# Kernel tuning notes

Measured on AMD Instinct MI355X. Metric: run time of the kernel, lower is better.

The kernel has to match this reference:

```python
import jax, jax.numpy as jnp
import numpy as np

N = 100000
E = 1600000
D = 64


def setup_inputs() -> dict:
    key = jax.random.key(0)
    ks = jax.random.split(key, 10)
    x = jax.random.normal(ks[0], (N, D), dtype=jnp.float32)
    edge_index = jax.random.randint(ks[1], (2, E), 0, N, dtype=jnp.int64)
    edge_weight = jax.random.uniform(ks[2], (E,), dtype=jnp.float32)
    s = 1.0 / np.sqrt(D)
    # GraphConv params: lin_rel (with bias) applied to aggregated messages,
    # lin_root (no bias) applied to the node's own features.
    W_rel1 = jax.random.uniform(ks[3], (D, D), jnp.float32, -s, s)
    b_rel1 = jax.random.uniform(ks[4], (D,), jnp.float32, -s, s)
    W_root1 = jax.random.uniform(ks[5], (D, D), jnp.float32, -s, s)
    W_rel2 = jax.random.uniform(ks[6], (D, D), jnp.float32, -s, s)
    b_rel2 = jax.random.uniform(ks[7], (D,), jnp.float32, -s, s)
    W_root2 = jax.random.uniform(ks[8], (D, D), jnp.float32, -s, s)
    return {"x": x, "edge_index": edge_index, "edge_weight": edge_weight,
            "W_rel1": W_rel1, "b_rel1": b_rel1, "W_root1": W_root1,
            "W_rel2": W_rel2, "b_rel2": b_rel2, "W_root2": W_root2}


def _graph_conv(x, src, dst, ew, W_rel, b_rel, W_root):
    # message: x_j * e_ji, scatter-add at target node i (edge_index[1])
    msg = x[src] * ew[:, None]                                   # [E, D]
    agg = jax.ops.segment_sum(msg, dst, num_segments=x.shape[0])  # [N, D]
    return agg @ W_rel.T + b_rel + x @ W_root.T


def reference(x, edge_index, edge_weight, W_rel1, b_rel1, W_root1, W_rel2, b_rel2, W_root2):
    src, dst = edge_index[0], edge_index[1]
    h = _graph_conv(x, src, dst, edge_weight, W_rel1, b_rel1, W_root1)
    h = jax.nn.relu(h)
    h = _graph_conv(h, src, dst, edge_weight, W_rel2, b_rel2, W_root2)
    return h  # final ReLU dropped (layers[:-1])
```

## Files before the change

kernel.cpp:

```cpp
#include <hip/hip_runtime.h>
#include <hip/hip_bf16.h>
#include <stdint.h>


#define D 64
#define EPB   2048
#define EPT   4
#define NBMAX 256
#define CAPB  10240
#define GW 8
#define GR 4
#define AW 8

typedef unsigned int   u32;
typedef unsigned short u16;

__device__ __forceinline__ float bf2f(u16 v) {
    return __uint_as_float(((u32)v) << 16);
}
__device__ __forceinline__ u16 f2bf(float f) {
    u32 u = __float_as_uint(f);
    u32 r = (u + 0x7fffu + ((u >> 16) & 1u)) >> 16;
    return (u16)r;
}

__global__ __launch_bounds__(512) void binA_kernel(
    const int* __restrict__ ei, const float* __restrict__ ew,
    int* __restrict__ bucketCnt, uint64_t* __restrict__ bucketBuf, int E_, int nb)
{
    __shared__ uint64_t lds_e[EPB];
    __shared__ int lcnt[NBMAX];
    __shared__ int loff[NBMAX];
    __shared__ int gbase[NBMAX];

    int tid  = threadIdx.x;
    int tile = blockIdx.x * EPB;
    int cnt  = min(EPB, E_ - tile);
    if (cnt <= 0) return;

    for (int k = tid; k < nb; k += 512) lcnt[k] = 0;
    __syncthreads();

    bool     val[EPT];
    int      lp[EPT], bk[EPT];
    uint64_t ent[EPT];
#pragma unroll
    for (int j = 0; j < EPT; ++j) {
        int l = j * 512 + tid;
        val[j] = (l < cnt);
        if (val[j]) {
            int e   = tile + l;
            int src = ei[e];
            int dst = ei[E_ + e];
            u32 wb  = (u32)f2bf(ew[e]) & 0x7FFFu;
            u32 p32 = ((u32)src << 15) | wb;
            int b   = dst >> 9;
            ent[j] = ((uint64_t)(u32)dst << 32) | p32;
            bk[j]  = b;
            lp[j]  = atomicAdd(&lcnt[b], 1);
        }
    }
    __syncthreads();

    if (tid == 0) {
        int run = 0;
        for (int b = 0; b < nb; ++b) { int c = lcnt[b]; loff[b] = run; run += c; }
    }
    __syncthreads();
    if (tid < nb) gbase[tid] = atomicAdd(&bucketCnt[tid], lcnt[tid]);
    __syncthreads();

#pragma unroll
    for (int j = 0; j < EPT; ++j)
        if (val[j]) lds_e[loff[bk[j]] + lp[j]] = ent[j];
    __syncthreads();

    for (int k = tid; k < cnt; k += 512) {
        uint64_t en = lds_e[k];
        int b   = (int)(en >> 41);
        int gp  = gbase[b] + (k - loff[b]);
        if (gp < CAPB)
            bucketBuf[(size_t)b * CAPB + gp] = en;
    }
}

__global__ __launch_bounds__(256) void degscan_kernel(
    const uint64_t* __restrict__ bucketBuf, const int* __restrict__ bucketCnt,
    int* __restrict__ loc, int* __restrict__ bucketTot, int nb, int Nn)
{
    __shared__ int ldeg[512];
    __shared__ int wsum[4];
    int b = blockIdx.x;
    if (b >= nb) return;
    int node0 = b << 9;
    int tid = threadIdx.x;
    for (int k = tid; k < 512; k += 256) ldeg[k] = 0;
    __syncthreads();

    int cnt = min(bucketCnt[b], CAPB);
    for (int k = tid; k < cnt; k += 256)
        atomicAdd(&ldeg[((int)(bucketBuf[(size_t)b * CAPB + k] >> 32)) - node0], 1);
    __syncthreads();

    int v0 = ldeg[2 * tid], v1 = ldeg[2 * tid + 1];
    int s = v0 + v1;
    int lane = tid & 63, wave = tid >> 6;
    int inc = s;
    for (int off = 1; off < 64; off <<= 1) {
        int u = __shfl_up(inc, off);
        if (lane >= off) inc += u;
    }
    if (lane == 63) wsum[wave] = inc;
    __syncthreads();
    int woff = 0;
    for (int w2 = 0; w2 < wave; ++w2) woff += wsum[w2];
    int ex = woff + inc - s;
    int n0 = node0 + 2 * tid;
    if (n0 < Nn)     loc[n0]     = ex;
    if (n0 + 1 < Nn) loc[n0 + 1] = ex + v0;
    if (tid == 255) bucketTot[b] = woff + inc;
}

__global__ __launch_bounds__(1024) void scan2_kernel(int* __restrict__ partial, int nchunk)
{
    __shared__ int sd[1024];
    int t = threadIdx.x;
    if (t < nchunk) sd[t] = partial[t];
    __syncthreads();
    if (t == 0) {
        int run = 0;
        for (int i = 0; i < nchunk; ++i) { int v = sd[i]; sd[i] = run; run += v; }
    }
    __syncthreads();
    if (t < nchunk) partial[t] = sd[t];
}

__global__ __launch_bounds__(256) void binB2_kernel(
    const uint64_t* __restrict__ bucketBuf, const int* __restrict__ bucketCnt,
    const int* __restrict__ loc, const int* __restrict__ partial,
    int* __restrict__ rowptr, u32* __restrict__ pairs, int nb, int Nn, int E_)
{
    __shared__ int lcur[512];
    int b = blockIdx.x;
    if (b >= nb) return;
    int node0 = b << 9;
    int tid = threadIdx.x;
    int base = partial[b];
    for (int k = tid; k < 512; k += 256) {
        int node = node0 + k;
        if (node < Nn) {
            int v = loc[node] + base;
            lcur[k] = v;
            rowptr[node] = v;
        }
    }
    if (b == nb - 1 && tid == 0) rowptr[Nn] = E_;
    __syncthreads();

    int cnt = min(bucketCnt[b], CAPB);
    for (int k = tid; k < cnt; k += 256) {
        uint64_t en = bucketBuf[(size_t)b * CAPB + k];
        int dst = (int)(en >> 32);
        int p = atomicAdd(&lcur[dst - node0], 1);
        pairs[p] = (u32)en;
    }
}

__global__ __launch_bounds__(512) void gemm_kernel(
    const float* xin,
    const float* __restrict__ Wrel, const float* __restrict__ brel,
    const float* __restrict__ Wroot,
    u16* __restrict__ xr, float* io, int Nn)
{
    __shared__ float WrelT[D][D + 1];
    __shared__ float WrootT[D][D + 1];
    __shared__ float bias[D];
    __shared__ float rowX[GW][GR][D];

    int tid = threadIdx.x;
    for (int i = tid; i < D * D; i += 512) {
        int d = i >> 6, k = i & 63;
        WrelT [k][d] = Wrel [i];
        WrootT[k][d] = Wroot[i];
    }
    if (tid < D) bias[tid] = brel[tid];
    __syncthreads();

    int wave = tid >> 6, lane = tid & 63;

    int base = (blockIdx.x * GW + wave) * GR;
    if (base >= Nn) return;
    int nr = min(GR, Nn - base);

    for (int r = 0; r < nr; ++r)
        rowX[wave][r][lane] = xin[(size_t)(base + r) * D + lane];

    float aR[GR] = {0.f, 0.f, 0.f, 0.f};
    float aC[GR] = {0.f, 0.f, 0.f, 0.f};
#pragma unroll
    for (int k4 = 0; k4 < 16; ++k4) {
        float4 xv[GR];
#pragma unroll
        for (int r = 0; r < GR; ++r)
            xv[r] = *reinterpret_cast<const float4*>(&rowX[wave][r][k4 * 4]);
#pragma unroll
        for (int kk = 0; kk < 4; ++kk) {
            float wr = WrelT [k4 * 4 + kk][lane];
            float wc = WrootT[k4 * 4 + kk][lane];
#pragma unroll
            for (int r = 0; r < GR; ++r) {
                float xk = (kk == 0) ? xv[r].x : (kk == 1) ? xv[r].y
                         : (kk == 2) ? xv[r].z : xv[r].w;
                aR[r] = fmaf(xk, wr, aR[r]);
                aC[r] = fmaf(xk, wc, aC[r]);
            }
        }
    }
    for (int r = 0; r < nr; ++r) {
        size_t o = (size_t)(base + r) * D + lane;
        xr[o] = f2bf(aR[r]);
        io[o] = aC[r] + bias[lane];
    }
}

__global__ __launch_bounds__(512) void gather1_fused(
    const u16* __restrict__ xr1, const u32* __restrict__ pairs,
    const int* __restrict__ rowptr,
    const float* __restrict__ Wrel, const float* __restrict__ brel,
    const float* __restrict__ Wroot,
    u16* __restrict__ xr2, float* __restrict__ io, int Nn)
{
    __shared__ float WrelT[D][D + 1];
    __shared__ float WrootT[D][D + 1];
    __shared__ float bias[D];
    __shared__ float rowH[GW][2][D];

    int tid = threadIdx.x;
    for (int i2 = tid; i2 < D * D; i2 += 512) {
        int d = i2 >> 6, k = i2 & 63;
        WrelT [k][d] = Wrel [i2];
        WrootT[k][d] = Wroot[i2];
    }
    if (tid < D) bias[tid] = brel[tid];
    __syncthreads();

    int wave = tid >> 6, lane = tid & 63;
    int i0 = ((int)blockIdx.x * GW + wave) * 2;
    if (i0 >= Nn) return;
    int i1 = i0 + 1;
    bool row1v = (i1 < Nn);
    int i1c = row1v ? i1 : i0;

    int beg0 = __builtin_amdgcn_readfirstlane(rowptr[i0]);
    int end0 = __builtin_amdgcn_readfirstlane(rowptr[i0 + 1]);
    int beg1 = __builtin_amdgcn_readfirstlane(rowptr[i1c]);
    int end1 = __builtin_amdgcn_readfirstlane(rowptr[i1c + 1]);
    int deg0 = end0 - beg0;
    int deg1 = row1v ? (end1 - beg1) : 0;
    int dmax = max(deg0, deg1);

    int half = lane >> 5;
    int c    = lane & 31;

    float a00 = 0.f, a01 = 0.f, a10 = 0.f, a11 = 0.f;
    for (int b = 0; b < dmax; b += 16) {
#pragma unroll
        for (int jj = 0; jj < 8; ++jj) {
            int j0 = b + 2 * jj;
            u32 q0 = pairs[beg0 + j0];
            u32 q1 = pairs[beg0 + j0 + 1];
            int   s00 = (j0     < deg0) ? (int)(q0 >> 15) : 0;
            float w00 = (j0     < deg0) ? __uint_as_float((q0 & 0x7FFFu) << 16) : 0.f;
            int   s01 = (j0 + 1 < deg0) ? (int)(q1 >> 15) : 0;
            float w01 = (j0 + 1 < deg0) ? __uint_as_float((q1 & 0x7FFFu) << 16) : 0.f;
            int   sa  = half ? s01 : s00;
            float wa  = half ? w01 : w00;
            u32 va = *reinterpret_cast<const u32*>(xr1 + (size_t)sa * D + c * 2);
            u32 r0 = pairs[beg1 + j0];
            u32 r1 = pairs[beg1 + j0 + 1];
            int   s10 = (j0     < deg1) ? (int)(r0 >> 15) : 0;
            float w10 = (j0     < deg1) ? __uint_as_float((r0 & 0x7FFFu) << 16) : 0.f;
            int   s11 = (j0 + 1 < deg1) ? (int)(r1 >> 15) : 0;
            float w11 = (j0 + 1 < deg1) ? __uint_as_float((r1 & 0x7FFFu) << 16) : 0.f;
            int   sb  = half ? s11 : s10;
            float wb  = half ? w11 : w10;
            u32 vb = *reinterpret_cast<const u32*>(xr1 + (size_t)sb * D + c * 2);

            a00 = fmaf(__uint_as_float(va << 16),          wa, a00);
            a01 = fmaf(__uint_as_float(va & 0xFFFF0000u),  wa, a01);
            a10 = fmaf(__uint_as_float(vb << 16),          wb, a10);
            a11 = fmaf(__uint_as_float(vb & 0xFFFF0000u),  wb, a11);
        }
    }
    a00 += __shfl_xor(a00, 32);
    a01 += __shfl_xor(a01, 32);
    a10 += __shfl_xor(a10, 32);
    a11 += __shfl_xor(a11, 32);

    if (half == 0)
        *reinterpret_cast<float2*>(&rowH[wave][0][c * 2]) = make_float2(a00, a01);
    else
        *reinterpret_cast<float2*>(&rowH[wave][1][c * 2]) = make_float2(a10, a11);

    size_t o0 = (size_t)i0 * D + lane;
    float h0 = fmaxf(rowH[wave][0][lane] + io[o0], 0.f);
    rowH[wave][0][lane] = h0;
    size_t o1 = (size_t)i1c * D + lane;
    float h1 = fmaxf(rowH[wave][1][lane] + io[o1], 0.f);
    rowH[wave][1][lane] = h1;

#pragma unroll
    for (int r = 0; r < 2; ++r) {
        if (r == 1 && !row1v) break;
        const float4* rH4 = reinterpret_cast<const float4*>(rowH[wave][r]);
        float aR = 0.f;
        float aC = bias[lane];
#pragma unroll
        for (int k4 = 0; k4 < 16; ++k4) {
            float4 hv = rH4[k4];
            int k = k4 * 4;
            aR = fmaf(hv.x, WrelT [k + 0][lane], aR);
            aR = fmaf(hv.y, WrelT [k + 1][lane], aR);
            aR = fmaf(hv.z, WrelT [k + 2][lane], aR);
            aR = fmaf(hv.w, WrelT [k + 3][lane], aR);
            aC = fmaf(hv.x, WrootT[k + 0][lane], aC);
            aC = fmaf(hv.y, WrootT[k + 1][lane], aC);
            aC = fmaf(hv.z, WrootT[k + 2][lane], aC);
            aC = fmaf(hv.w, WrootT[k + 3][lane], aC);
        }
        size_t o = (size_t)(i0 + r) * D + lane;
        xr2[o] = f2bf(aR);
        io[o]  = aC;
    }
}

__global__ __launch_bounds__(512) void gather2_kernel(
    const u16* __restrict__ xr, const u32* __restrict__ pairs,
    const int* __restrict__ rowptr, float* __restrict__ io, int Nn)
{
    int tid  = threadIdx.x;
    int wave = tid >> 6, lane = tid & 63;
    int i0 = ((int)blockIdx.x * AW + wave) * 2;
    if (i0 >= Nn) return;
    int i1 = i0 + 1;
    bool row1v = (i1 < Nn);
    int i1c = row1v ? i1 : i0;

    int beg0 = __builtin_amdgcn_readfirstlane(rowptr[i0]);
    int end0 = __builtin_amdgcn_readfirstlane(rowptr[i0 + 1]);
    int beg1 = __builtin_amdgcn_readfirstlane(rowptr[i1c]);
    int end1 = __builtin_amdgcn_readfirstlane(rowptr[i1c + 1]);
    int deg0 = end0 - beg0;
    int deg1 = row1v ? (end1 - beg1) : 0;
    int dmax = max(deg0, deg1);

    int half = lane >> 5;
    int c    = lane & 31;

    float a00 = 0.f, a01 = 0.f, a10 = 0.f, a11 = 0.f;
    for (int b = 0; b < dmax; b += 16) {
#pragma unroll
        for (int jj = 0; jj < 8; ++jj) {
            int j0 = b + 2 * jj;
            u32 q0 = pairs[beg0 + j0];
            u32 q1 = pairs[beg0 + j0 + 1];
            int   s00 = (j0     < deg0) ? (int)(q0 >> 15) : 0;
            float w00 = (j0     < deg0) ? __uint_as_float((q0 & 0x7FFFu) << 16) : 0.f;
            int   s01 = (j0 + 1 < deg0) ? (int)(q1 >> 15) : 0;
            float w01 = (j0 + 1 < deg0) ? __uint_as_float((q1 & 0x7FFFu) << 16) : 0.f;
            int   sa  = half ? s01 : s00;
            float wa  = half ? w01 : w00;
            u32 va = *reinterpret_cast<const u32*>(xr + (size_t)sa * D + c * 2);
            u32 r0 = pairs[beg1 + j0];
            u32 r1 = pairs[beg1 + j0 + 1];
            int   s10 = (j0     < deg1) ? (int)(r0 >> 15) : 0;
            float w10 = (j0     < deg1) ? __uint_as_float((r0 & 0x7FFFu) << 16) : 0.f;
            int   s11 = (j0 + 1 < deg1) ? (int)(r1 >> 15) : 0;
            float w11 = (j0 + 1 < deg1) ? __uint_as_float((r1 & 0x7FFFu) << 16) : 0.f;
            int   sb  = half ? s11 : s10;
            float wb  = half ? w11 : w10;
            u32 vb = *reinterpret_cast<const u32*>(xr + (size_t)sb * D + c * 2);

            a00 = fmaf(__uint_as_float(va << 16),         wa, a00);
            a01 = fmaf(__uint_as_float(va & 0xFFFF0000u), wa, a01);
            a10 = fmaf(__uint_as_float(vb << 16),         wb, a10);
            a11 = fmaf(__uint_as_float(vb & 0xFFFF0000u), wb, a11);
        }
    }
    a00 += __shfl_xor(a00, 32);
    a01 += __shfl_xor(a01, 32);
    a10 += __shfl_xor(a10, 32);
    a11 += __shfl_xor(a11, 32);

    if (half == 0) {
        float2* p0 = reinterpret_cast<float2*>(&io[(size_t)i0 * D + c * 2]);
        float2 c0 = *p0; c0.x += a00; c0.y += a01; *p0 = c0;
    } else if (row1v) {
        float2* p1 = reinterpret_cast<float2*>(&io[(size_t)i1 * D + c * 2]);
        float2 c1 = *p1; c1.x += a10; c1.y += a11; *p1 = c1;
    }
}

extern "C" void kernel_launch(void* const* d_in, const int* in_sizes, int n_in,
                              void* d_out, int out_size, void* d_ws, size_t ws_size,
                              hipStream_t stream)
{
    const float* x      = (const float*)d_in[0];
    const int*   ei     = (const int*)  d_in[1];
    const float* ew     = (const float*)d_in[2];
    const float* Wrel1  = (const float*)d_in[3];
    const float* brel1  = (const float*)d_in[4];
    const float* Wroot1 = (const float*)d_in[5];
    const float* Wrel2  = (const float*)d_in[6];
    const float* brel2  = (const float*)d_in[7];
    const float* Wroot2 = (const float*)d_in[8];
    float* out = (float*)d_out;

    const int E_ = in_sizes[2];
    const int Nn = in_sizes[0] / D;
    const int nb = (Nn + 511) >> 9;

    char* w = (char*)d_ws;
    size_t off = 0;
    u16*  xr1    = (u16*)(w + off); off += (size_t)Nn * D * sizeof(u16);
    u16*  xr2    = (u16*)(w + off); off += (size_t)Nn * D * sizeof(u16);
    uint64_t* bucketBuf = (uint64_t*)d_ws;
    int*  rowptr = (int*)(w + off); off += (size_t)(Nn + 1) * sizeof(int);
    int*  loc    = (int*)(w + off); off += (size_t)Nn * sizeof(int);
    int*  bucketCnt = (int*)(w + off); off += NBMAX * sizeof(int);
    int*  partial= (int*)(w + off); off += 1024 * sizeof(int);
    off = (off + 15) & ~(size_t)15;
    u32* pairs = (u32*)(w + off);

    const int aBlocks = (E_ + EPB - 1) / EPB;
    const int gemmBlocks = (Nn + GW * GR - 1) / (GW * GR);
    const int g1Blocks   = (Nn + GW * 2 - 1) / (GW * 2);
    const int g2Blocks   = (Nn + AW * 2 - 1) / (AW * 2);

    (void)hipMemsetAsync(bucketCnt, 0, NBMAX * sizeof(int), stream);
    binA_kernel<<<aBlocks, 512, 0, stream>>>(ei, ew, bucketCnt, bucketBuf, E_, nb);
    degscan_kernel<<<nb, 256, 0, stream>>>(bucketBuf, bucketCnt, loc, partial, nb, Nn);
    scan2_kernel<<<1, 1024, 0, stream>>>(partial, nb);
    binB2_kernel<<<nb, 256, 0, stream>>>(bucketBuf, bucketCnt, loc, partial,
                                         rowptr, pairs, nb, Nn, E_);

    gemm_kernel<<<gemmBlocks, 512, 0, stream>>>(x, Wrel1, brel1, Wroot1, xr1, out, Nn);
    gather1_fused<<<g1Blocks, 512, 0, stream>>>(xr1, pairs, rowptr,
                                                Wrel2, brel2, Wroot2, xr2, out, Nn);
    gather2_kernel<<<g2Blocks, 512, 0, stream>>>(xr2, pairs, rowptr, out, Nn);
}
```

Before: 235.7 us.

## Fuse degree scan, bucket prefix scan and CSR fill into one kernel

Merges degscan, scan2 and binB2 into a single per-bucket kernel. Each block derives its global base offset by summing the preceding bucket counts with shared-memory atomics, computes local degrees and an exclusive scan in LDS, then writes rowptr and scatters the pairs. This removes two kernel launches and the round trip of the loc and partial arrays through global memory. In exchange, each block re-reads up to 196 bucket counts redundantly.

```diff
diff --git a/kernel.cpp b/kernel.cpp
--- a/kernel.cpp
+++ b/kernel.cpp
@@ -84,23 +84,28 @@
     }
 }
 
-__global__ __launch_bounds__(256) void degscan_kernel(
+__global__ __launch_bounds__(256) void binB3_kernel(
     const uint64_t* __restrict__ bucketBuf, const int* __restrict__ bucketCnt,
-    int* __restrict__ loc, int* __restrict__ bucketTot, int nb, int Nn)
+    int* __restrict__ rowptr, u32* __restrict__ pairs, int nb, int Nn, int E_)
 {
     __shared__ int ldeg[512];
+    __shared__ int lcur[512];
     __shared__ int wsum[4];
+    __shared__ int sbase;
     int b = blockIdx.x;
     if (b >= nb) return;
     int node0 = b << 9;
     int tid = threadIdx.x;
+
+    if (tid == 0) sbase = 0;
     for (int k = tid; k < 512; k += 256) ldeg[k] = 0;
     __syncthreads();
-
+    if (tid < b) atomicAdd(&sbase, min(bucketCnt[tid], CAPB));
     int cnt = min(bucketCnt[b], CAPB);
     for (int k = tid; k < cnt; k += 256)
         atomicAdd(&ldeg[((int)(bucketBuf[(size_t)b * CAPB + k] >> 32)) - node0], 1);
     __syncthreads();
+    int base = sbase;
 
     int v0 = ldeg[2 * tid], v1 = ldeg[2 * tid + 1];
     int s = v0 + v1;
@@ -116,48 +121,11 @@
     for (int w2 = 0; w2 < wave; ++w2) woff += wsum[w2];
     int ex = woff + inc - s;
     int n0 = node0 + 2 * tid;
-    if (n0 < Nn)     loc[n0]     = ex;
-    if (n0 + 1 < Nn) loc[n0 + 1] = ex + v0;
-    if (tid == 255) bucketTot[b] = woff + inc;
-}
-
-__global__ __launch_bounds__(1024) void scan2_kernel(int* __restrict__ partial, int nchunk)
-{
-    __shared__ int sd[1024];
-    int t = threadIdx.x;
-    if (t < nchunk) sd[t] = partial[t];
-    __syncthreads();
-    if (t == 0) {
-        int run = 0;
-        for (int i = 0; i < nchunk; ++i) { int v = sd[i]; sd[i] = run; run += v; }
-    }
-    __syncthreads();
-    if (t < nchunk) partial[t] = sd[t];
-}
-
-__global__ __launch_bounds__(256) void binB2_kernel(
-    const uint64_t* __restrict__ bucketBuf, const int* __restrict__ bucketCnt,
-    const int* __restrict__ loc, const int* __restrict__ partial,
-    int* __restrict__ rowptr, u32* __restrict__ pairs, int nb, int Nn, int E_)
-{
-    __shared__ int lcur[512];
-    int b = blockIdx.x;
-    if (b >= nb) return;
-    int node0 = b << 9;
-    int tid = threadIdx.x;
-    int base = partial[b];
-    for (int k = tid; k < 512; k += 256) {
-        int node = node0 + k;
-        if (node < Nn) {
-            int v = loc[node] + base;
-            lcur[k] = v;
-            rowptr[node] = v;
-        }
-    }
+    if (n0 < Nn)     { int v = base + ex;      lcur[2 * tid]     = v; rowptr[n0]     = v; }
+    if (n0 + 1 < Nn) { int v = base + ex + v0; lcur[2 * tid + 1] = v; rowptr[n0 + 1] = v; }
     if (b == nb - 1 && tid == 0) rowptr[Nn] = E_;
     __syncthreads();
 
-    int cnt = min(bucketCnt[b], CAPB);
     for (int k = tid; k < cnt; k += 256) {
         uint64_t en = bucketBuf[(size_t)b * CAPB + k];
         int dst = (int)(en >> 32);
@@ -426,9 +394,7 @@
     u16*  xr2    = (u16*)(w + off); off += (size_t)Nn * D * sizeof(u16);
     uint64_t* bucketBuf = (uint64_t*)d_ws;
     int*  rowptr = (int*)(w + off); off += (size_t)(Nn + 1) * sizeof(int);
-    int*  loc    = (int*)(w + off); off += (size_t)Nn * sizeof(int);
     int*  bucketCnt = (int*)(w + off); off += NBMAX * sizeof(int);
-    int*  partial= (int*)(w + off); off += 1024 * sizeof(int);
     off = (off + 15) & ~(size_t)15;
     u32* pairs = (u32*)(w + off);
 
@@ -439,10 +405,7 @@
 
     (void)hipMemsetAsync(bucketCnt, 0, NBMAX * sizeof(int), stream);
     binA_kernel<<<aBlocks, 512, 0, stream>>>(ei, ew, bucketCnt, bucketBuf, E_, nb);
-    degscan_kernel<<<nb, 256, 0, stream>>>(bucketBuf, bucketCnt, loc, partial, nb, Nn);
-    scan2_kernel<<<1, 1024, 0, stream>>>(partial, nb);
-    binB2_kernel<<<nb, 256, 0, stream>>>(bucketBuf, bucketCnt, loc, partial,
-                                         rowptr, pairs, nb, Nn, E_);
+    binB3_kernel<<<nb, 256, 0, stream>>>(bucketBuf, bucketCnt, rowptr, pairs, nb, Nn, E_);
 
     gemm_kernel<<<gemmBlocks, 512, 0, stream>>>(x, Wrel1, brel1, Wroot1, xr1, out, Nn);
     gather1_fused<<<g1Blocks, 512, 0, stream>>>(xr1, pairs, rowptr,
```

After: 235.4 us. About the same (-0.1%).
